# Kernel tuning notes

Measured on AMD Instinct MI355X. Metric: run time of the kernel, lower is better.

## Reference

```python
import jax, jax.numpy as jnp
import numpy as np

H = 768; NH = 12; DH = H // NH; E = 2; R = 128; B = 32; S = 512
SCALE = 1.0 / np.sqrt(DH)


def _mha_core(q, k, v, mask):
    # q,k,v: [B,S,H] projected; mask: [B,S] (1 = keep)
    b, s, _ = q.shape
    qh = q.reshape(b, s, NH, DH)
    kh = k.reshape(b, s, NH, DH)
    vh = v.reshape(b, s, NH, DH)
    scores = jnp.einsum('bqhd,bkhd->bhqk', qh, kh) * SCALE
    scores = scores + (1.0 - mask)[:, None, None, :] * (-10000.0)
    probs = jax.nn.softmax(scores, axis=-1)
    return jnp.einsum('bhqk,bkhd->bqhd', probs, vh).reshape(b, s, H)


def _forward(x, switch_w, switch_b, c_wq, c_bq, c_wk, c_bk, c_wv, c_bv, c_wo, c_bo,
             e_wq, e_bq, e_aq, e_gq, e_wk, e_bk, e_ak, e_gk, e_wv, e_bv, e_av, e_gv,
             e_wo, e_bo, attention_mask):
    # --- switch routing (per-sample, mean-pooled over sequence) ---
    logits = x.mean(axis=1) @ switch_w + switch_b          # [B,E]
    route_prob = jax.nn.softmax(logits, axis=-1)
    route_prob_max = route_prob.max(axis=-1)               # [B]
    routes = jnp.argmax(route_prob, axis=-1)               # [B]
    onehot = jax.nn.one_hot(routes, E, dtype=x.dtype)      # [B,E] dense equivalent of gather/scatter dispatch

    # --- LoRA attention experts (vmapped over experts) ---
    def lora_expert(wq, bq, aq, gq, wk, bk, ak, gk, wv, bv, av, gv, wo, bo):
        q = x @ wq + bq + (x @ aq) @ gq
        k = x @ wk + bk + (x @ ak) @ gk
        v = x @ wv + bv + (x @ av) @ gv
        return _mha_core(q, k, v, attention_mask) @ wo + bo   # [B,S,H]

    expert_out = jax.vmap(lora_expert)(e_wq, e_bq, e_aq, e_gq, e_wk, e_bk, e_ak, e_gk,
                                       e_wv, e_bv, e_av, e_gv, e_wo, e_bo)  # [E,B,S,H]
    routed = jnp.einsum('ebsh,be->bsh', expert_out, onehot)

    # scaling factor = p_max / stop_grad(p_max) (forward identity, grad path to router)
    scaling = (route_prob_max / jax.lax.stop_gradient(route_prob_max))[:, None, None]
    routed = routed * scaling

    # --- common (shared) attention expert ---
    q = x @ c_wq + c_bq
    k = x @ c_wk + c_bk
    v = x @ c_wv + c_bv
    common = _mha_core(q, k, v, attention_mask) @ c_wo + c_bo
    return routed + common


def setup_inputs() -> dict:
    key = jax.random.key(0)
    ks = jax.random.split(key, 32)
    std = 0.02
    def w(i, shape):
        return jax.random.normal(ks[i], shape, jnp.float32) * std
    z = lambda shape: jnp.zeros(shape, jnp.float32)
    return {
        'x': jax.random.normal(ks[0], (B, S, H), jnp.float32),
        'switch_w': w(1, (H, E)), 'switch_b': z((E,)),
        'c_wq': w(2, (H, H)), 'c_bq': z((H,)),
        'c_wk': w(3, (H, H)), 'c_bk': z((H,)),
        'c_wv': w(4, (H, H)), 'c_bv': z((H,)),
        'c_wo': w(5, (H, H)), 'c_bo': z((H,)),
        'e_wq': w(6, (E, H, H)), 'e_bq': z((E, H)),
        'e_aq': w(7, (E, H, R)), 'e_gq': w(8, (E, R, H)),
        'e_wk': w(9, (E, H, H)), 'e_bk': z((E, H)),
        'e_ak': w(10, (E, H, R)), 'e_gk': w(11, (E, R, H)),
        'e_wv': w(12, (E, H, H)), 'e_bv': z((E, H)),
        'e_av': w(13, (E, H, R)), 'e_gv': w(14, (E, R, H)),
        'e_wo': w(15, (E, H, H)), 'e_bo': z((E, H)),
        'attention_mask': jnp.ones((B, S), jnp.float32),
    }


def reference(x, switch_w, switch_b, c_wq, c_bq, c_wk, c_bk, c_wv, c_bv, c_wo, c_bo,
              e_wq, e_bq, e_aq, e_gq, e_wk, e_bk, e_ak, e_gk, e_wv, e_bv, e_av, e_gv,
              e_wo, e_bo, attention_mask):
    return _forward(x, switch_w, switch_b, c_wq, c_bq, c_wk, c_bk, c_wv, c_bv, c_wo, c_bo,
                    e_wq, e_bq, e_aq, e_gq, e_wk, e_bk, e_ak, e_gk, e_wv, e_bv, e_av, e_gv,
                    e_wo, e_bo, attention_mask)
```

## Files before the change

### kernel.cpp

```cpp
#include <hip/hip_runtime.h>
#include <hip/hip_bf16.h>

#define DEVINL __device__ __forceinline__

typedef __bf16 bf16x8 __attribute__((ext_vector_type(8)));
typedef float f32x4 __attribute__((ext_vector_type(4)));
typedef unsigned short u16x8 __attribute__((ext_vector_type(8)));
typedef unsigned short u16x4 __attribute__((ext_vector_type(4)));

DEVINL unsigned short f2bf(float f) {
  __hip_bfloat16 h = __float2bfloat16(f);
  return __builtin_bit_cast(unsigned short, h);
}

DEVINL float bf2f(unsigned short u) {
  return __builtin_bit_cast(float, ((unsigned)u) << 16);
}

DEVINL f32x4 mfma16(bf16x8 a, bf16x8 b, f32x4 c) {
  return __builtin_amdgcn_mfma_f32_16x16x32_bf16(a, b, c, 0, 0, 0);
}

DEVINL void gload_lds16(const void* g, void* l) {
  __builtin_amdgcn_global_load_lds(
      (const __attribute__((address_space(1))) unsigned int*)g,
      (__attribute__((address_space(3))) unsigned int*)l, 16, 0, 0);
}

__global__ __launch_bounds__(256) void k_cvt(const float* __restrict__ x,
                                             u16x8* __restrict__ xb) {
  int i = blockIdx.x * 256 + threadIdx.x;
  const float* p = x + (size_t)i * 8;
  float4 a = *(const float4*)p;
  float4 b = *(const float4*)(p + 4);
  u16x8 o;
  o[0] = f2bf(a.x); o[1] = f2bf(a.y); o[2] = f2bf(a.z); o[3] = f2bf(a.w);
  o[4] = f2bf(b.x); o[5] = f2bf(b.y); o[6] = f2bf(b.z); o[7] = f2bf(b.w);
  xb[i] = o;
}

__global__ __launch_bounds__(256) void k_xsum(const float* __restrict__ x,
                                              float* __restrict__ xsum) {
  int b = blockIdx.x, sc = blockIdx.z;
  int h = blockIdx.y * 256 + threadIdx.x;
  float s = 0.f;
  const float* p = x + ((size_t)(b * 512 + sc * 128)) * 768 + h;
  for (int i = 0; i < 128; ++i) s += p[(size_t)i * 768];
  xsum[(sc * 32 + b) * 768 + h] = s;
}

__global__ __launch_bounds__(256) void k_route(const float* __restrict__ xsum,
                                               const float* __restrict__ sw,
                                               const float* __restrict__ sb,
                                               int* __restrict__ route) {
  int b = blockIdx.x, t = threadIdx.x;
  float l0 = 0.f, l1 = 0.f;
  for (int h = t; h < 768; h += 256) {
    float xm = (xsum[(0 * 32 + b) * 768 + h] + xsum[(1 * 32 + b) * 768 + h] +
                xsum[(2 * 32 + b) * 768 + h] + xsum[(3 * 32 + b) * 768 + h]) *
               (1.f / 512.f);
    l0 += xm * sw[h * 2 + 0];
    l1 += xm * sw[h * 2 + 1];
  }
#pragma unroll
  for (int off = 32; off; off >>= 1) {
    l0 += __shfl_down(l0, off);
    l1 += __shfl_down(l1, off);
  }
  __shared__ float s0[4], s1[4];
  int w = t >> 6;
  if ((t & 63) == 0) { s0[w] = l0; s1[w] = l1; }
  __syncthreads();
  if (t == 0) {
    float a0 = sb[0] + s0[0] + s0[1] + s0[2] + s0[3];
    float a1 = sb[1] + s1[0] + s1[1] + s1[2] + s1[3];
    route[b] = (a1 > a0) ? 1 : 0;
  }
}

__global__ __launch_bounds__(256) void k_wt(const float* __restrict__ cwq, const float* __restrict__ cwk,
                                            const float* __restrict__ cwv, const float* __restrict__ cwo,
                                            const float* __restrict__ ewo,
                                            const float* __restrict__ ewq, const float* __restrict__ ewk,
                                            const float* __restrict__ ewv,
                                            unsigned short* __restrict__ wtc,
                                            unsigned short* __restrict__ wtewo,
                                            unsigned short* __restrict__ wtexp) {
  __shared__ float t[32][33];
  int z = blockIdx.z;
  const float* src;
  unsigned short* dst;
  if (z < 4) {
    src = (z == 0) ? cwq : (z == 1) ? cwk : (z == 2) ? cwv : cwo;
    dst = wtc + (size_t)z * 589824;
  } else if (z < 6) {
    src = ewo + (size_t)(z - 4) * 589824;
    dst = wtewo + (size_t)(z - 4) * 589824;
  } else {
    int mat = (z - 6) >> 1, e = (z - 6) & 1;
    src = ((mat == 0) ? ewq : (mat == 1) ? ewk : ewv) + (size_t)e * 589824;
    dst = wtexp + (size_t)(mat * 2 + e) * 589824;
  }
  int k0 = blockIdx.x * 32, n0 = blockIdx.y * 32;
  int tid = threadIdx.x;
#pragma unroll
  for (int i = 0; i < 4; ++i) {
    int lin = tid + 256 * i; int kk = lin >> 5, nn = lin & 31;
    t[kk][nn] = src[(size_t)(k0 + kk) * 768 + n0 + nn];
  }
  __syncthreads();
#pragma unroll
  for (int i = 0; i < 4; ++i) {
    int lin = tid + 256 * i; int nn = lin >> 5, kk = lin & 31;
    dst[(size_t)(n0 + nn) * 768 + k0 + kk] = f2bf(t[kk][nn]);
  }
}

__global__ __launch_bounds__(256) void k_acvt(const float* __restrict__ eaq, const float* __restrict__ eak,
                                              const float* __restrict__ eav,
                                              unsigned short* __restrict__ abt) {
  int z = blockIdx.z;
  int mat = z >> 1, e = z & 1;
  const float* src = ((mat == 0) ? eaq : (mat == 1) ? eak : eav) + (size_t)e * 98304;
  unsigned short* dst = abt + (size_t)z * 98304;
  int i = blockIdx.x * 256 + threadIdx.x;
  const float* p = src + (size_t)i * 8;
  float4 a = *(const float4*)p;
  float4 b = *(const float4*)(p + 4);
  u16x8 o;
  o[0] = f2bf(a.x); o[1] = f2bf(a.y); o[2] = f2bf(a.z); o[3] = f2bf(a.w);
  o[4] = f2bf(b.x); o[5] = f2bf(b.y); o[6] = f2bf(b.z); o[7] = f2bf(b.w);
  *(u16x8*)(dst + (size_t)i * 8) = o;
}

__global__ __launch_bounds__(256) void k_gtr(const float* __restrict__ egq, const float* __restrict__ egk,
                                             const float* __restrict__ egv,
                                             unsigned short* __restrict__ gtb) {
  __shared__ float t[32][33];
  int z = blockIdx.z;
  int mat = z >> 1, e = z & 1;
  const float* src = ((mat == 0) ? egq : (mat == 1) ? egk : egv) + (size_t)e * 98304;
  unsigned short* dst = gtb + (size_t)z * 98304;
  int n0 = blockIdx.x * 32, r0 = blockIdx.y * 32;
  int tid = threadIdx.x;
#pragma unroll
  for (int i = 0; i < 4; ++i) {
    int lin = tid + 256 * i; int rr = lin >> 5, nn = lin & 31;
    t[rr][nn] = src[(size_t)(r0 + rr) * 768 + n0 + nn];
  }
  __syncthreads();
#pragma unroll
  for (int i = 0; i < 4; ++i) {
    int lin = tid + 256 * i; int nn = lin >> 5, rr = lin & 31;
    dst[(size_t)(n0 + nn) * 128 + r0 + rr] = f2bf(t[rr][nn]);
  }
}

__global__ __launch_bounds__(256) void k_mergemm(const unsigned short* __restrict__ gtb,
                                                 const unsigned short* __restrict__ abt,
                                                 const unsigned short* __restrict__ wtexp,
                                                 unsigned short* __restrict__ wte) {
  const int z = blockIdx.z;
  const int m0 = blockIdx.x * 128, n0 = blockIdx.y * 128;
  const unsigned short* Am = gtb + (size_t)z * 98304;
  const unsigned short* Bm = abt + (size_t)z * 98304;
  const unsigned short* Wt = wtexp + (size_t)z * 589824;
  unsigned short* dst = wte + (size_t)z * 589824;
  __shared__ __align__(16) unsigned short As[128 * 32];
  __shared__ __align__(16) unsigned short Bs[128 * 32];
  const int tid = threadIdx.x, w = tid >> 6, lane = tid & 63, g = lane >> 4, l15 = lane & 15;
  const int wr = (w >> 1) * 64, wc = (w & 1) * 64;
  f32x4 acc[4][4] = {};
  for (int k0 = 0; k0 < 128; k0 += 32) {
#pragma unroll
    for (int c = 0; c < 2; ++c) {
      int o = (w * 2 + c) * 1024 + lane * 16;
      int row = o >> 6, chunk = (o >> 4) & 3;
      gload_lds16(Am + (size_t)(m0 + row) * 128 + k0 + (chunk << 3),
                  (char*)As + (w * 2 + c) * 1024);
      gload_lds16(Bm + (size_t)(n0 + row) * 128 + k0 + (chunk << 3),
                  (char*)Bs + (w * 2 + c) * 1024);
    }
    __syncthreads();
    bf16x8 af[4], bfr[4];
#pragma unroll
    for (int mi = 0; mi < 4; ++mi) {
      int row = wr + mi * 16 + l15;
      af[mi] = *(const bf16x8*)((const char*)As + row * 64 + (g << 4));
    }
#pragma unroll
    for (int ni = 0; ni < 4; ++ni) {
      int row = wc + ni * 16 + l15;
      bfr[ni] = *(const bf16x8*)((const char*)Bs + row * 64 + (g << 4));
    }
#pragma unroll
    for (int mi = 0; mi < 4; ++mi)
#pragma unroll
      for (int ni = 0; ni < 4; ++ni)
        acc[mi][ni] = mfma16(af[mi], bfr[ni], acc[mi][ni]);
    __syncthreads();
  }
#pragma unroll
  for (int ni = 0; ni < 4; ++ni) {
    int col = n0 + wc + ni * 16 + l15;
#pragma unroll
    for (int mi = 0; mi < 4; ++mi) {
#pragma unroll
      for (int r = 0; r < 4; ++r) {
        int row = m0 + wr + mi * 16 + 4 * g + r;
        size_t idx = (size_t)row * 768 + col;
        dst[idx] = f2bf(acc[mi][ni][r] + bf2f(Wt[idx]));
      }
    }
  }
}

template <int MH, int KK, bool LOADB>
DEVINL void qphase(const unsigned short* As, const unsigned short* Bs,
                   bf16x8 (&bfr)[4], f32x4 (&acc)[8][4],
                   int wr, int wc, int g, int l15) {
  if (LOADB) {
#pragma unroll
    for (int nj = 0; nj < 4; ++nj) {
      int row = wc + nj * 16 + l15;
      bfr[nj] = *(const bf16x8*)((const char*)Bs + row * 128 + (((KK * 4 + g) ^ (row & 7)) << 4));
    }
  }
  bf16x8 af[4];
#pragma unroll
  for (int mi = 0; mi < 4; ++mi) {
    int row = wr + MH * 64 + mi * 16 + l15;
    af[mi] = *(const bf16x8*)((const char*)As + row * 128 + (((KK * 4 + g) ^ (row & 7)) << 4));
  }
  __builtin_amdgcn_s_setprio(1);
#pragma unroll
  for (int mi = 0; mi < 4; ++mi)
#pragma unroll
    for (int nj = 0; nj < 4; ++nj)
      acc[MH * 4 + mi][nj] = mfma16(af[mi], bfr[nj], acc[MH * 4 + mi][nj]);
  __builtin_amdgcn_s_setprio(0);
}

__global__ __launch_bounds__(512, 2) void k_gemm_qkv(
    const unsigned short* __restrict__ xb, const unsigned short* __restrict__ wtc,
    const unsigned short* __restrict__ wte,
    const float* __restrict__ cbq, const float* __restrict__ cbk, const float* __restrict__ cbv,
    const float* __restrict__ ebq, const float* __restrict__ ebk, const float* __restrict__ ebv,
    const int* __restrict__ route,
    unsigned short* __restrict__ outq, unsigned short* __restrict__ outk,
    unsigned short* __restrict__ vt, int expert) {
  extern __shared__ __align__(16) unsigned short smem[];
  const int m0 = blockIdx.x * 256, n0 = blockIdx.y * 256, mat = blockIdx.z;
  const int b = m0 >> 9;
  const unsigned short* wt;
  const float* bias;
  if (!expert) {
    wt = wtc + (size_t)mat * 589824;
    bias = (mat == 0) ? cbq : (mat == 1) ? cbk : cbv;
  } else {
    int e = route[b];
    wt = wte + (size_t)(mat * 2 + e) * 589824;
    bias = ((mat == 0) ? ebq : (mat == 1) ? ebk : ebv) + e * 768;
  }
  const int tid = threadIdx.x, w = tid >> 6, lane = tid & 63, g = lane >> 4, l15 = lane & 15;
  const int wr = (w >> 2) * 128, wc = (w & 3) * 64;
  const int srow = lane >> 3, sslot = lane & 7;
  f32x4 acc[8][4] = {};

  auto stage_half = [&](int buf, int t, int h) {
    const unsigned short* src = (h < 2) ? xb : wt;
    int rowbase = (h < 2) ? (m0 + h * 128) : (n0 + (h - 2) * 128);
    unsigned short* lb = smem + buf * 32768 + ((h < 2) ? (h * 8192) : (16384 + (h - 2) * 8192));
    int k0 = t * 64;
#pragma unroll
    for (int c = 0; c < 2; ++c) {
      int rl = (w * 2 + c) * 8 + srow;
      int gc = (sslot ^ (rl & 7)) << 3;
      gload_lds16(src + (size_t)(rowbase + rl) * 768 + k0 + gc,
                  (char*)lb + (w * 2 + c) * 1024);
    }
  };

#pragma unroll
  for (int h = 0; h < 4; ++h) stage_half(0, 0, h);
  int cur = 0;
  for (int t = 0; t < 12; ++t) {
    const int nxt = cur ^ 1;
    const int tn = (t + 1 < 12) ? (t + 1) : 0;
    const unsigned short* As = smem + cur * 32768;
    const unsigned short* Bs = smem + cur * 32768 + 16384;
    bf16x8 bfr[4];
    stage_half(nxt, tn, 0);
    stage_half(nxt, tn, 2);
    asm volatile("s_waitcnt vmcnt(4)" ::: "memory");
    asm volatile("s_barrier" ::: "memory");
    qphase<0, 0, true>(As, Bs, bfr, acc, wr, wc, g, l15);
    stage_half(nxt, tn, 1);
    stage_half(nxt, tn, 3);
    asm volatile("s_barrier" ::: "memory");
    qphase<1, 0, false>(As, Bs, bfr, acc, wr, wc, g, l15);
    asm volatile("s_barrier" ::: "memory");
    qphase<0, 1, true>(As, Bs, bfr, acc, wr, wc, g, l15);
    asm volatile("s_barrier" ::: "memory");
    qphase<1, 1, false>(As, Bs, bfr, acc, wr, wc, g, l15);
    asm volatile("s_barrier" ::: "memory");
    cur = nxt;
  }
  __syncthreads();

  if (mat != 2) {
    unsigned short* pw = smem + w * 8192;
#pragma unroll
    for (int nj = 0; nj < 4; ++nj) {
      float bv = bias[n0 + wc + nj * 16 + l15];
#pragma unroll
      for (int fr = 0; fr < 8; ++fr)
#pragma unroll
        for (int r = 0; r < 4; ++r) {
          int lr = fr * 16 + 4 * g + r;
          int lc = nj * 16 + l15;
          pw[lr * 64 + (((lc >> 3) ^ (lr & 7)) << 3) + (lc & 7)] =
              f2bf(acc[fr][nj][r] + bv);
        }
    }
    unsigned short* dst = (mat == 0) ? outq : outk;
#pragma unroll
    for (int i = 0; i < 16; ++i) {
      int ci = i * 64 + lane;
      int row = ci >> 3;
      int c8 = ci & 7;
      u16x8 v = *(const u16x8*)(pw + row * 64 + ((c8 ^ (row & 7)) << 3));
      *(u16x8*)(dst + (size_t)(m0 + wr + row) * 768 + n0 + wc + c8 * 8) = v;
    }
  } else {
    unsigned short* Ts2 = smem;
#pragma unroll
    for (int p = 0; p < 2; ++p) {
      if (((w & 3) >> 1) == p) {
#pragma unroll
        for (int nj = 0; nj < 4; ++nj) {
          int ccl = ((w & 3) & 1) * 64 + nj * 16 + l15;
          float bv = bias[n0 + p * 128 + ccl];
#pragma unroll
          for (int fr = 0; fr < 8; ++fr)
#pragma unroll
            for (int r = 0; r < 4; ++r) {
              int row = wr + fr * 16 + 4 * g + r;
              Ts2[ccl * 264 + row] = f2bf(acc[fr][nj][r] + bv);
            }
        }
      }
      __syncthreads();
#pragma unroll
      for (int i = 0; i < 8; ++i) {
        int ci = tid + 512 * i, cc = ci >> 5, j = ci & 31;
        u16x8 v = *(const u16x8*)(Ts2 + cc * 264 + j * 8);
        int colg = n0 + p * 128 + cc;
        int head = colg >> 6, dh = colg & 63;
        *(u16x8*)(vt + ((size_t)((b * 12 + head) * 64 + dh)) * 512 + (m0 & 511) + j * 8) = v;
      }
      __syncthreads();
    }
  }
}

__global__ __launch_bounds__(512) void k_attn(
    const unsigned short* __restrict__ Q, const unsigned short* __restrict__ K,
    const unsigned short* __restrict__ Vt, const float* __restrict__ mask,
    unsigned short* __restrict__ ctx) {
  const int qh = blockIdx.x, h = blockIdx.y, b = blockIdx.z;
  const int tid = threadIdx.x, w = tid >> 6, lane = tid & 63, g = lane >> 4, l15 = lane & 15;
  const int qbase = b * 512 + qh * 256 + w * 32;
  bf16x8 qf[2][2];
#pragma unroll
  for (int qs = 0; qs < 2; ++qs) {
    const unsigned short* qp = Q + (size_t)(qbase + qs * 16 + l15) * 768 + h * 64;
    qf[qs][0] = *(const bf16x8*)(qp + g * 8);
    qf[qs][1] = *(const bf16x8*)(qp + 32 + g * 8);
  }
  __shared__ __align__(16) unsigned short Ks[64 * 64];
  __shared__ __align__(16) unsigned short Vs[64 * 64];
  __shared__ __align__(16) unsigned short Pl[8 * 16 * 64];
  __shared__ float mk2[64];
  float lsum[2] = {0.f, 0.f};
  f32x4 acc[2][4] = {};
  const unsigned short* Kb = K + (size_t)(b * 512) * 768 + h * 64;
  const unsigned short* Vb = Vt + (size_t)((b * 12 + h) * 64) * 512;
  unsigned short* pws = Pl + w * 1024;
  const int srow = w * 8 + (lane >> 3);
  const int schunk = lane & 7;
  const int ssw = (schunk ^ (srow & 7)) << 3;
  const float C = 0.125f * 1.44269504f;
  for (int kt = 0; kt < 8; ++kt) {
    const int kv0 = kt * 64;
    gload_lds16(Kb + (size_t)(kv0 + srow) * 768 + ssw, (char*)Ks + w * 1024);
    gload_lds16(Vb + (size_t)srow * 512 + kv0 + ssw, (char*)Vs + w * 1024);
    if (tid < 64) mk2[tid] = (1.f - mask[b * 512 + kv0 + tid]) * (-14426.9504f);
    __syncthreads();
#pragma unroll
    for (int qs = 0; qs < 2; ++qs) {
      f32x4 sf[4];
#pragma unroll
      for (int mb = 0; mb < 4; ++mb) {
        int row = mb * 16 + l15;
        bf16x8 ka  = *(const bf16x8*)(Ks + row * 64 + ((g ^ (row & 7)) << 3));
        bf16x8 kb2 = *(const bf16x8*)(Ks + row * 64 + (((g + 4) ^ (row & 7)) << 3));
        f32x4 z = {0.f, 0.f, 0.f, 0.f};
        z = mfma16(ka, qf[qs][0], z);
        z = mfma16(kb2, qf[qs][1], z);
        sf[mb] = z;
      }
      float p[16];
      float psum = 0.f;
#pragma unroll
      for (int mb = 0; mb < 4; ++mb)
#pragma unroll
        for (int r = 0; r < 4; ++r) {
          float e2 = exp2f(fmaf(sf[mb][r], C, mk2[mb * 16 + g * 4 + r]));
          p[mb * 4 + r] = e2;
          psum += e2;
        }
      lsum[qs] += psum;
#pragma unroll
      for (int mb = 0; mb < 4; ++mb)
#pragma unroll
        for (int hh = 0; hh < 2; ++hh) {
          unsigned val = (unsigned)f2bf(p[mb * 4 + 2 * hh]) |
                         ((unsigned)f2bf(p[mb * 4 + 2 * hh + 1]) << 16);
          int off = mb * 16 + 4 * g + 2 * hh;
          int cw = (off >> 3) ^ (l15 & 7);
          *(unsigned*)(pws + l15 * 64 + (cw << 3) + (off & 7)) = val;
        }
#pragma unroll
      for (int ks = 0; ks < 2; ++ks) {
        bf16x8 pf = *(const bf16x8*)(pws + l15 * 64 + (((4 * ks + g) ^ (l15 & 7)) << 3));
#pragma unroll
        for (int d = 0; d < 4; ++d) {
          int row = d * 16 + l15;
          bf16x8 vf = *(const bf16x8*)(Vs + row * 64 + (((g + 4 * ks) ^ (row & 7)) << 3));
          acc[qs][d] = mfma16(vf, pf, acc[qs][d]);
        }
      }
    }
    __syncthreads();
  }
#pragma unroll
  for (int qs = 0; qs < 2; ++qs) {
    float t = lsum[qs];
    t += __shfl_xor(t, 16);
    t += __shfl_xor(t, 32);
    float inv = 1.f / t;
    unsigned short* op = ctx + (size_t)(qbase + qs * 16 + l15) * 768 + h * 64;
#pragma unroll
    for (int d = 0; d < 4; ++d) {
      u16x4 o4;
#pragma unroll
      for (int r = 0; r < 4; ++r) o4[r] = f2bf(acc[qs][d][r] * inv);
      *(u16x4*)(op + d * 16 + 4 * g) = o4;
    }
  }
}

__global__ __launch_bounds__(256) void k_gemm_out(
    const unsigned short* __restrict__ ctxc, const unsigned short* __restrict__ ctxe,
    const unsigned short* __restrict__ woc, const unsigned short* __restrict__ woe,
    const float* __restrict__ cbo, const float* __restrict__ ebo,
    const int* __restrict__ route, float* __restrict__ out) {
  const int m0 = blockIdx.x * 128, n0 = blockIdx.y * 128;
  const int b = m0 >> 9;
  const int e = route[b];
  __shared__ __align__(16) unsigned short smem2[128 * 128];
  unsigned short* As = smem2;
  unsigned short* Bs = smem2 + 8192;
  const int tid = threadIdx.x, w = tid >> 6, lane = tid & 63, g = lane >> 4, l15 = lane & 15;
  const int wr = (w >> 1) * 64, wc = (w & 1) * 64;
  const int srow = (lane >> 3);
  const int sslot = lane & 7;
  f32x4 acc[4][4] = {};
  for (int k0 = 0; k0 < 1536; k0 += 64) {
    const unsigned short* asrc = (k0 < 768) ? ctxc : ctxe;
    const unsigned short* wsrc = (k0 < 768) ? woc : (woe + (size_t)e * 589824);
    const int kk0 = (k0 < 768) ? k0 : (k0 - 768);
#pragma unroll
    for (int c = 0; c < 4; ++c) {
      int row = (w * 4 + c) * 8 + srow;
      int gc = (sslot ^ (row & 7)) << 3;
      gload_lds16(asrc + (size_t)(m0 + row) * 768 + kk0 + gc, (char*)As + (w * 4 + c) * 1024);
      gload_lds16(wsrc + (size_t)(n0 + row) * 768 + kk0 + gc, (char*)Bs + (w * 4 + c) * 1024);
    }
    __syncthreads();
#pragma unroll
    for (int kk = 0; kk < 2; ++kk) {
      bf16x8 af[4], bfr[4];
#pragma unroll
      for (int mi = 0; mi < 4; ++mi) {
        int row = wr + mi * 16 + l15;
        af[mi] = *(const bf16x8*)((const char*)As + row * 128 + (((kk * 4 + g) ^ (row & 7)) << 4));
      }
#pragma unroll
      for (int ni = 0; ni < 4; ++ni) {
        int row = wc + ni * 16 + l15;
        bfr[ni] = *(const bf16x8*)((const char*)Bs + row * 128 + (((kk * 4 + g) ^ (row & 7)) << 4));
      }
#pragma unroll
      for (int mi = 0; mi < 4; ++mi)
#pragma unroll
        for (int ni = 0; ni < 4; ++ni)
          acc[mi][ni] = mfma16(af[mi], bfr[ni], acc[mi][ni]);
    }
    __syncthreads();
  }
  float* fs = (float*)smem2;
#pragma unroll
  for (int p = 0; p < 2; ++p) {
    if ((w >> 1) == p) {
#pragma unroll
      for (int ni = 0; ni < 4; ++ni) {
        int col = n0 + wc + ni * 16 + l15;
        float bsum = cbo[col] + ebo[e * 768 + col];
#pragma unroll
        for (int mi = 0; mi < 4; ++mi)
#pragma unroll
          for (int r = 0; r < 4; ++r) {
            int lr = mi * 16 + 4 * g + r;
            int lc = wc + ni * 16 + l15;
            fs[lr * 128 + (((lc >> 2) ^ (lr & 7)) << 2) + (lc & 3)] =
                acc[mi][ni][r] + bsum;
          }
      }
    }
    __syncthreads();
#pragma unroll
    for (int j = 0; j < 8; ++j) {
      int ci = j * 256 + tid;
      int row = ci >> 5;
      int sl = ci & 31;
      f32x4 v = *(const f32x4*)(fs + row * 128 + ((sl ^ (row & 7)) << 2));
      *(f32x4*)(out + (size_t)(m0 + p * 64 + row) * 768 + n0 + sl * 4) = v;
    }
    __syncthreads();
  }
}

extern "C" void kernel_launch(void* const* d_in, const int* in_sizes, int n_in,
                              void* d_out, int out_size, void* d_ws, size_t ws_size,
                              hipStream_t stream) {
  const float* x    = (const float*)d_in[0];
  const float* sw   = (const float*)d_in[1];
  const float* sb   = (const float*)d_in[2];
  const float* cwq  = (const float*)d_in[3];
  const float* cbq  = (const float*)d_in[4];
  const float* cwk  = (const float*)d_in[5];
  const float* cbk  = (const float*)d_in[6];
  const float* cwv  = (const float*)d_in[7];
  const float* cbv  = (const float*)d_in[8];
  const float* cwo  = (const float*)d_in[9];
  const float* cbo  = (const float*)d_in[10];
  const float* ewq  = (const float*)d_in[11];
  const float* ebq  = (const float*)d_in[12];
  const float* eaq  = (const float*)d_in[13];
  const float* egq  = (const float*)d_in[14];
  const float* ewk  = (const float*)d_in[15];
  const float* ebk  = (const float*)d_in[16];
  const float* eak  = (const float*)d_in[17];
  const float* egk  = (const float*)d_in[18];
  const float* ewv  = (const float*)d_in[19];
  const float* ebv  = (const float*)d_in[20];
  const float* eav  = (const float*)d_in[21];
  const float* egv  = (const float*)d_in[22];
  const float* ewo  = (const float*)d_in[23];
  const float* ebo  = (const float*)d_in[24];
  const float* amask = (const float*)d_in[25];
  (void)in_sizes; (void)n_in; (void)out_size; (void)ws_size; (void)amask;

  (void)hipFuncSetAttribute(reinterpret_cast<const void*>(k_gemm_qkv),
                            hipFuncAttributeMaxDynamicSharedMemorySize, 131072);

  char* ws = (char*)d_ws;
  const size_t SZ = 25165824;
  unsigned short* xb    = (unsigned short*)(ws);
  unsigned short* ctxe  = (unsigned short*)(ws);
  unsigned short* qb    = (unsigned short*)(ws + SZ);
  unsigned short* kbuf  = (unsigned short*)(ws + 2 * SZ);
  unsigned short* vt    = (unsigned short*)(ws + 3 * SZ);
  unsigned short* ctxc  = (unsigned short*)(ws + 4 * SZ);
  unsigned short* wtc   = (unsigned short*)(ws + 5 * SZ);
  unsigned short* wte   = (unsigned short*)(ws + 5 * SZ + 4718592);
  unsigned short* wtewo = (unsigned short*)(ws + 5 * SZ + 4718592 + 7077888);
  float* xsum           = (float*)(ws + 5 * SZ + 4718592 + 7077888 + 2359296);
  int* route            = (int*)(ws + 5 * SZ + 4718592 + 7077888 + 2359296 + 393216);
  unsigned short* abt   = (unsigned short*)(ws + SZ);
  unsigned short* gtb   = (unsigned short*)(ws + SZ + 1179648);
  unsigned short* wtexp = (unsigned short*)(ws + SZ + 2359296);

  k_cvt<<<6144, 256, 0, stream>>>(x, (u16x8*)xb);
  k_xsum<<<dim3(32, 3, 4), 256, 0, stream>>>(x, xsum);
  k_route<<<32, 256, 0, stream>>>(xsum, sw, sb, route);
  k_wt<<<dim3(24, 24, 12), 256, 0, stream>>>(cwq, cwk, cwv, cwo, ewo, ewq, ewk, ewv,
                                             wtc, wtewo, wtexp);
  k_acvt<<<dim3(48, 1, 6), 256, 0, stream>>>(eaq, eak, eav, abt);
  k_gtr<<<dim3(24, 4, 6), 256, 0, stream>>>(egq, egk, egv, gtb);
  k_mergemm<<<dim3(6, 6, 6), 256, 0, stream>>>(gtb, abt, wtexp, wte);
  k_gemm_qkv<<<dim3(64, 3, 3), 512, 131072, stream>>>(xb, wtc, wte, cbq, cbk, cbv,
                                                      ebq, ebk, ebv, route, qb, kbuf, vt, 0);
  k_attn<<<dim3(2, 12, 32), 512, 0, stream>>>(qb, kbuf, vt, amask, ctxc);
  k_gemm_qkv<<<dim3(64, 3, 3), 512, 131072, stream>>>(xb, wtc, wte, cbq, cbk, cbv,
                                                      ebq, ebk, ebv, route, qb, kbuf, vt, 1);
  k_attn<<<dim3(2, 12, 32), 512, 0, stream>>>(qb, kbuf, vt, amask, ctxe);
  k_gemm_out<<<dim3(128, 6), 256, 0, stream>>>(ctxc, ctxe, wtc + 3 * 589824, wtewo,
                                               cbo, ebo, route, (float*)d_out);
}
```

Baseline: 390.3 us.

## Merge common and expert QKV/attention launches and retile output GEMM

When the workspace is large enough, the common and expert QKV projections and attention run as single launches with doubled grids. Each path gets its own Q/K/V buffers, so one launch does the work of two. Separately, the output projection GEMM moves to 256x256 tiles with 512 threads, double-buffered LDS staging, and the same qphase pipeline the QKV GEMM uses. The aim is less launch serialisation, fuller waves, and better operand reuse. The trade-offs are a larger workspace requirement and only 192 output-GEMM blocks, which may under-fill the GPU.

```diff
diff --git a/kernel.cpp b/kernel.cpp
--- a/kernel.cpp
+++ b/kernel.cpp
@@ -247,10 +247,13 @@
     const float* __restrict__ cbq, const float* __restrict__ cbk, const float* __restrict__ cbv,
     const float* __restrict__ ebq, const float* __restrict__ ebk, const float* __restrict__ ebv,
     const int* __restrict__ route,
-    unsigned short* __restrict__ outq, unsigned short* __restrict__ outk,
-    unsigned short* __restrict__ vt, int expert) {
+    unsigned short* __restrict__ qC, unsigned short* __restrict__ kC, unsigned short* __restrict__ vC,
+    unsigned short* __restrict__ qE, unsigned short* __restrict__ kE, unsigned short* __restrict__ vE,
+    int base_expert) {
   extern __shared__ __align__(16) unsigned short smem[];
-  const int m0 = blockIdx.x * 256, n0 = blockIdx.y * 256, mat = blockIdx.z;
+  const int m0 = blockIdx.x * 256, n0 = blockIdx.y * 256;
+  const int mat = blockIdx.z % 3;
+  const int expert = base_expert + blockIdx.z / 3;
   const int b = m0 >> 9;
   const unsigned short* wt;
   const float* bias;
@@ -262,6 +265,9 @@
     wt = wte + (size_t)(mat * 2 + e) * 589824;
     bias = ((mat == 0) ? ebq : (mat == 1) ? ebk : ebv) + e * 768;
   }
+  unsigned short* outq = expert ? qE : qC;
+  unsigned short* outk = expert ? kE : kC;
+  unsigned short* vt   = expert ? vE : vC;
   const int tid = threadIdx.x, w = tid >> 6, lane = tid & 63, g = lane >> 4, l15 = lane & 15;
   const int wr = (w >> 2) * 128, wc = (w & 3) * 64;
   const int srow = lane >> 3, sslot = lane & 7;
@@ -365,10 +371,17 @@
 }
 
 __global__ __launch_bounds__(512) void k_attn(
-    const unsigned short* __restrict__ Q, const unsigned short* __restrict__ K,
-    const unsigned short* __restrict__ Vt, const float* __restrict__ mask,
-    unsigned short* __restrict__ ctx) {
-  const int qh = blockIdx.x, h = blockIdx.y, b = blockIdx.z;
+    const unsigned short* __restrict__ Q0, const unsigned short* __restrict__ K0,
+    const unsigned short* __restrict__ V0, unsigned short* __restrict__ ctx0,
+    const unsigned short* __restrict__ Q1, const unsigned short* __restrict__ K1,
+    const unsigned short* __restrict__ V1, unsigned short* __restrict__ ctx1,
+    const float* __restrict__ mask) {
+  const int qh = blockIdx.x, h = blockIdx.y;
+  const int b = blockIdx.z & 31, path = blockIdx.z >> 5;
+  const unsigned short* Q = path ? Q1 : Q0;
+  const unsigned short* K = path ? K1 : K0;
+  const unsigned short* Vt = path ? V1 : V0;
+  unsigned short* ctx = path ? ctx1 : ctx0;
   const int tid = threadIdx.x, w = tid >> 6, lane = tid & 63, g = lane >> 4, l15 = lane & 15;
   const int qbase = b * 512 + qh * 256 + w * 32;
   bf16x8 qf[2][2];
@@ -461,81 +474,90 @@
   }
 }
 
-__global__ __launch_bounds__(256) void k_gemm_out(
+__global__ __launch_bounds__(512, 2) void k_gemm_out(
     const unsigned short* __restrict__ ctxc, const unsigned short* __restrict__ ctxe,
     const unsigned short* __restrict__ woc, const unsigned short* __restrict__ woe,
     const float* __restrict__ cbo, const float* __restrict__ ebo,
     const int* __restrict__ route, float* __restrict__ out) {
-  const int m0 = blockIdx.x * 128, n0 = blockIdx.y * 128;
+  extern __shared__ __align__(16) unsigned short smem[];
+  const int m0 = blockIdx.x * 256, n0 = blockIdx.y * 256;
   const int b = m0 >> 9;
   const int e = route[b];
-  __shared__ __align__(16) unsigned short smem2[128 * 128];
-  unsigned short* As = smem2;
-  unsigned short* Bs = smem2 + 8192;
   const int tid = threadIdx.x, w = tid >> 6, lane = tid & 63, g = lane >> 4, l15 = lane & 15;
-  const int wr = (w >> 1) * 64, wc = (w & 1) * 64;
-  const int srow = (lane >> 3);
-  const int sslot = lane & 7;
-  f32x4 acc[4][4] = {};
-  for (int k0 = 0; k0 < 1536; k0 += 64) {
-    const unsigned short* asrc = (k0 < 768) ? ctxc : ctxe;
-    const unsigned short* wsrc = (k0 < 768) ? woc : (woe + (size_t)e * 589824);
-    const int kk0 = (k0 < 768) ? k0 : (k0 - 768);
-#pragma unroll
-    for (int c = 0; c < 4; ++c) {
-      int row = (w * 4 + c) * 8 + srow;
-      int gc = (sslot ^ (row & 7)) << 3;
-      gload_lds16(asrc + (size_t)(m0 + row) * 768 + kk0 + gc, (char*)As + (w * 4 + c) * 1024);
-      gload_lds16(wsrc + (size_t)(n0 + row) * 768 + kk0 + gc, (char*)Bs + (w * 4 + c) * 1024);
+  const int wr = (w >> 2) * 128, wc = (w & 3) * 64;
+  const int srow = lane >> 3, sslot = lane & 7;
+  f32x4 acc[8][4] = {};
+
+  auto stage_half = [&](int buf, int t, int h) {
+    const unsigned short* src =
+        (h < 2) ? ((t < 12) ? ctxc : ctxe)
+                : ((t < 12) ? woc : (woe + (size_t)e * 589824));
+    int rowbase = (h < 2) ? (m0 + h * 128) : (n0 + (h - 2) * 128);
+    unsigned short* lb = smem + buf * 32768 + ((h < 2) ? (h * 8192) : (16384 + (h - 2) * 8192));
+    int k0 = (t % 12) * 64;
+#pragma unroll
+    for (int c = 0; c < 2; ++c) {
+      int rl = (w * 2 + c) * 8 + srow;
+      int gc = (sslot ^ (rl & 7)) << 3;
+      gload_lds16(src + (size_t)(rowbase + rl) * 768 + k0 + gc,
+                  (char*)lb + (w * 2 + c) * 1024);
+    }
+  };
+
+#pragma unroll
+  for (int h = 0; h < 4; ++h) stage_half(0, 0, h);
+  int cur = 0;
+  for (int t = 0; t < 24; ++t) {
+    const int nxt = cur ^ 1;
+    const int tn = (t + 1 < 24) ? (t + 1) : 0;
+    const unsigned short* As = smem + cur * 32768;
+    const unsigned short* Bs = smem + cur * 32768 + 16384;
+    bf16x8 bfr[4];
+    stage_half(nxt, tn, 0);
+    stage_half(nxt, tn, 2);
+    asm volatile("s_waitcnt vmcnt(4)" ::: "memory");
+    asm volatile("s_barrier" ::: "memory");
+    qphase<0, 0, true>(As, Bs, bfr, acc, wr, wc, g, l15);
+    stage_half(nxt, tn, 1);
+    stage_half(nxt, tn, 3);
+    asm volatile("s_barrier" ::: "memory");
+    qphase<1, 0, false>(As, Bs, bfr, acc, wr, wc, g, l15);
+    asm volatile("s_barrier" ::: "memory");
+    qphase<0, 1, true>(As, Bs, bfr, acc, wr, wc, g, l15);
+    asm volatile("s_barrier" ::: "memory");
+    qphase<1, 1, false>(As, Bs, bfr, acc, wr, wc, g, l15);
+    asm volatile("s_barrier" ::: "memory");
+    cur = nxt;
+  }
+  __syncthreads();
+
+  float* fs = (float*)smem;
+#pragma unroll
+  for (int p = 0; p < 4; ++p) {
+    if ((w >> 2) == (p >> 1)) {
+#pragma unroll
+      for (int nj = 0; nj < 4; ++nj) {
+        int lc = wc + nj * 16 + l15;
+        int col = n0 + lc;
+        float bsum = cbo[col] + ebo[e * 768 + col];
+#pragma unroll
+        for (int fi = 0; fi < 4; ++fi) {
+          int fr = (p & 1) * 4 + fi;
+#pragma unroll
+          for (int r = 0; r < 4; ++r) {
+            int lr = fi * 16 + 4 * g + r;
+            fs[lr * 256 + (((lc >> 2) ^ (lr & 7)) << 2) + (lc & 3)] =
+                acc[fr][nj][r] + bsum;
+          }
+        }
+      }
     }
     __syncthreads();
 #pragma unroll
-    for (int kk = 0; kk < 2; ++kk) {
-      bf16x8 af[4], bfr[4];
-#pragma unroll
-      for (int mi = 0; mi < 4; ++mi) {
-        int row = wr + mi * 16 + l15;
-        af[mi] = *(const bf16x8*)((const char*)As + row * 128 + (((kk * 4 + g) ^ (row & 7)) << 4));
-      }
-#pragma unroll
-      for (int ni = 0; ni < 4; ++ni) {
-        int row = wc + ni * 16 + l15;
-        bfr[ni] = *(const bf16x8*)((const char*)Bs + row * 128 + (((kk * 4 + g) ^ (row & 7)) << 4));
-      }
-#pragma unroll
-      for (int mi = 0; mi < 4; ++mi)
-#pragma unroll
-        for (int ni = 0; ni < 4; ++ni)
-          acc[mi][ni] = mfma16(af[mi], bfr[ni], acc[mi][ni]);
-    }
-    __syncthreads();
-  }
-  float* fs = (float*)smem2;
-#pragma unroll
-  for (int p = 0; p < 2; ++p) {
-    if ((w >> 1) == p) {
-#pragma unroll
-      for (int ni = 0; ni < 4; ++ni) {
-        int col = n0 + wc + ni * 16 + l15;
-        float bsum = cbo[col] + ebo[e * 768 + col];
-#pragma unroll
-        for (int mi = 0; mi < 4; ++mi)
-#pragma unroll
-          for (int r = 0; r < 4; ++r) {
-            int lr = mi * 16 + 4 * g + r;
-            int lc = wc + ni * 16 + l15;
-            fs[lr * 128 + (((lc >> 2) ^ (lr & 7)) << 2) + (lc & 3)] =
-                acc[mi][ni][r] + bsum;
-          }
-      }
-    }
-    __syncthreads();
-#pragma unroll
     for (int j = 0; j < 8; ++j) {
-      int ci = j * 256 + tid;
-      int row = ci >> 5;
-      int sl = ci & 31;
-      f32x4 v = *(const f32x4*)(fs + row * 128 + ((sl ^ (row & 7)) << 2));
+      int ci = j * 512 + tid;
+      int row = ci >> 6, sl = ci & 63;
+      f32x4 v = *(const f32x4*)(fs + row * 256 + ((sl ^ (row & 7)) << 2));
       *(f32x4*)(out + (size_t)(m0 + p * 64 + row) * 768 + n0 + sl * 4) = v;
     }
     __syncthreads();
@@ -571,24 +593,45 @@
   const float* ewo  = (const float*)d_in[23];
   const float* ebo  = (const float*)d_in[24];
   const float* amask = (const float*)d_in[25];
-  (void)in_sizes; (void)n_in; (void)out_size; (void)ws_size; (void)amask;
+  (void)in_sizes; (void)n_in; (void)out_size;
 
   (void)hipFuncSetAttribute(reinterpret_cast<const void*>(k_gemm_qkv),
                             hipFuncAttributeMaxDynamicSharedMemorySize, 131072);
+  (void)hipFuncSetAttribute(reinterpret_cast<const void*>(k_gemm_out),
+                            hipFuncAttributeMaxDynamicSharedMemorySize, 131072);
 
   char* ws = (char*)d_ws;
   const size_t SZ = 25165824;
-  unsigned short* xb    = (unsigned short*)(ws);
-  unsigned short* ctxe  = (unsigned short*)(ws);
-  unsigned short* qb    = (unsigned short*)(ws + SZ);
-  unsigned short* kbuf  = (unsigned short*)(ws + 2 * SZ);
-  unsigned short* vt    = (unsigned short*)(ws + 3 * SZ);
-  unsigned short* ctxc  = (unsigned short*)(ws + 4 * SZ);
-  unsigned short* wtc   = (unsigned short*)(ws + 5 * SZ);
-  unsigned short* wte   = (unsigned short*)(ws + 5 * SZ + 4718592);
-  unsigned short* wtewo = (unsigned short*)(ws + 5 * SZ + 4718592 + 7077888);
-  float* xsum           = (float*)(ws + 5 * SZ + 4718592 + 7077888 + 2359296);
-  int* route            = (int*)(ws + 5 * SZ + 4718592 + 7077888 + 2359296 + 393216);
+  const size_t MERGED_NEED = 8 * SZ + 4718592 + 7077888 + 2359296 + 393216 + 256;
+  const bool merged = (ws_size >= MERGED_NEED);
+
+  unsigned short *xb, *qbC, *kC, *vC, *qbE, *kE, *vE, *ctxc, *ctxe;
+  char* wbase;
+  if (merged) {
+    xb   = (unsigned short*)(ws);
+    qbC  = (unsigned short*)(ws + SZ);
+    kC   = (unsigned short*)(ws + 2 * SZ);
+    vC   = (unsigned short*)(ws + 3 * SZ);
+    qbE  = (unsigned short*)(ws + 4 * SZ);
+    kE   = (unsigned short*)(ws + 5 * SZ);
+    vE   = (unsigned short*)(ws + 6 * SZ);
+    ctxc = (unsigned short*)(ws + 7 * SZ);
+    ctxe = (unsigned short*)(ws);
+    wbase = ws + 8 * SZ;
+  } else {
+    xb   = (unsigned short*)(ws);
+    qbC  = qbE = (unsigned short*)(ws + SZ);
+    kC   = kE  = (unsigned short*)(ws + 2 * SZ);
+    vC   = vE  = (unsigned short*)(ws + 3 * SZ);
+    ctxc = (unsigned short*)(ws + 4 * SZ);
+    ctxe = (unsigned short*)(ws);
+    wbase = ws + 5 * SZ;
+  }
+  unsigned short* wtc   = (unsigned short*)(wbase);
+  unsigned short* wte   = (unsigned short*)(wbase + 4718592);
+  unsigned short* wtewo = (unsigned short*)(wbase + 4718592 + 7077888);
+  float* xsum           = (float*)(wbase + 4718592 + 7077888 + 2359296);
+  int* route            = (int*)(wbase + 4718592 + 7077888 + 2359296 + 393216);
   unsigned short* abt   = (unsigned short*)(ws + SZ);
   unsigned short* gtb   = (unsigned short*)(ws + SZ + 1179648);
   unsigned short* wtexp = (unsigned short*)(ws + SZ + 2359296);
@@ -601,12 +644,25 @@
   k_acvt<<<dim3(48, 1, 6), 256, 0, stream>>>(eaq, eak, eav, abt);
   k_gtr<<<dim3(24, 4, 6), 256, 0, stream>>>(egq, egk, egv, gtb);
   k_mergemm<<<dim3(6, 6, 6), 256, 0, stream>>>(gtb, abt, wtexp, wte);
-  k_gemm_qkv<<<dim3(64, 3, 3), 512, 131072, stream>>>(xb, wtc, wte, cbq, cbk, cbv,
-                                                      ebq, ebk, ebv, route, qb, kbuf, vt, 0);
-  k_attn<<<dim3(2, 12, 32), 512, 0, stream>>>(qb, kbuf, vt, amask, ctxc);
-  k_gemm_qkv<<<dim3(64, 3, 3), 512, 131072, stream>>>(xb, wtc, wte, cbq, cbk, cbv,
-                                                      ebq, ebk, ebv, route, qb, kbuf, vt, 1);
-  k_attn<<<dim3(2, 12, 32), 512, 0, stream>>>(qb, kbuf, vt, amask, ctxe);
-  k_gemm_out<<<dim3(128, 6), 256, 0, stream>>>(ctxc, ctxe, wtc + 3 * 589824, wtewo,
-                                               cbo, ebo, route, (float*)d_out);
-}
+
+  if (merged) {
+    k_gemm_qkv<<<dim3(64, 3, 6), 512, 131072, stream>>>(
+        xb, wtc, wte, cbq, cbk, cbv, ebq, ebk, ebv, route,
+        qbC, kC, vC, qbE, kE, vE, 0);
+    k_attn<<<dim3(2, 12, 64), 512, 0, stream>>>(qbC, kC, vC, ctxc,
+                                                qbE, kE, vE, ctxe, amask);
+  } else {
+    k_gemm_qkv<<<dim3(64, 3, 3), 512, 131072, stream>>>(
+        xb, wtc, wte, cbq, cbk, cbv, ebq, ebk, ebv, route,
+        qbC, kC, vC, qbC, kC, vC, 0);
+    k_attn<<<dim3(2, 12, 32), 512, 0, stream>>>(qbC, kC, vC, ctxc,
+                                                qbC, kC, vC, ctxc, amask);
+    k_gemm_qkv<<<dim3(64, 3, 3), 512, 131072, stream>>>(
+        xb, wtc, wte, cbq, cbk, cbv, ebq, ebk, ebv, route,
+        qbC, kC, vC, qbC, kC, vC, 1);
+    k_attn<<<dim3(2, 12, 32), 512, 0, stream>>>(qbC, kC, vC, ctxe,
+                                                qbC, kC, vC, ctxe, amask);
+  }
+  k_gemm_out<<<dim3(64, 3), 512, 131072, stream>>>(ctxc, ctxe, wtc + 3 * 589824, wtewo,
+                                                   cbo, ebo, route, (float*)d_out);
+}
```

After: 349.4 us. -10.5%, faster.
